# Kernel tuning notes

Hardware: AMD Instinct MI355X
Metric: run time of the kernel (lower is better)

The kernel has to match this reference:

```python
import jax, jax.numpy as jnp
import numpy as np
import math

B, S, E, H = 4, 1024, 1024, 16
DK = E // H  # 64


def setup_inputs() -> dict:
    key = jax.random.key(0)
    ks = jax.random.split(key, 10)
    sc = 0.02
    inp = {
        "x": jax.random.normal(ks[0], (B, S, E), dtype=jnp.float32),
        "mask": jax.random.randint(ks[1], (B, S, S), 0, 2, dtype=jnp.int32),
        "Wq": jax.random.normal(ks[2], (E, E), dtype=jnp.float32) * sc,
        "bq": jnp.zeros((E,), dtype=jnp.float32),
        "Wk": jax.random.normal(ks[3], (E, E), dtype=jnp.float32) * sc,
        "bk": jnp.zeros((E,), dtype=jnp.float32),
        "Wv": jax.random.normal(ks[4], (E, E), dtype=jnp.float32) * sc,
        "bv": jnp.zeros((E,), dtype=jnp.float32),
        "Wo": jax.random.normal(ks[5], (E, E), dtype=jnp.float32) * sc,
        "bo": jnp.zeros((E,), dtype=jnp.float32),
    }
    return inp


def _split_heads(t):
    # [B, S, E] -> [B, H, S, DK]
    return t.reshape(B, S, H, DK).transpose(0, 2, 1, 3)


def reference(x, mask, Wq, bq, Wk, bk, Wv, bv, Wo, bo):
    # Linear projections (torch Linear: y = x @ W.T + b)
    q = _split_heads(x @ Wq.T + bq)
    k = _split_heads(x @ Wk.T + bk)
    v = _split_heads(x @ Wv.T + bv)  # computed but discarded, faithful to source bug
    # scores: [B, H, S, S]
    scores = jnp.einsum('bhqd,bhkd->bhqk', q, k) / jnp.float32(math.sqrt(DK))
    scores = jnp.where(mask[:, None, :, :] == 0, jnp.float32(-1e9), scores)
    scores = jax.nn.softmax(scores, axis=-1)
    # NOTE: source forward keeps dropout(scores) (eval mode -> identity) and
    # DISCARDS matmul(scores, v). We replicate that exactly.
    attn = scores  # [B, H, S, S]
    attn = attn.transpose(0, 2, 1, 3).reshape(B, -1, E)  # [B, S*S/DK, E]
    return attn @ Wo.T + bo
```

## Files before the change

### kernel.cpp

```cpp
#include <hip/hip_runtime.h>

typedef __bf16 bf16;
typedef __attribute__((ext_vector_type(8))) __bf16 bf16x8;
typedef __attribute__((ext_vector_type(4))) float f32x4;


__device__ __forceinline__ unsigned short f2bf(float f) {
    union { float f; unsigned u; } v; v.f = f;
    unsigned r = v.u + 0x7FFFu + ((v.u >> 16) & 1u);
    return (unsigned short)(r >> 16);
}

__device__ __forceinline__ void stage128x64(const bf16* g, int ld_elems,
                                            bf16* lds, int tid) {
    const char* gb = (const char*)g;
    const int ldb = ld_elems * 2;
#pragma unroll
    for (int r = 0; r < 4; ++r) {
        int lin = r * 256 + tid;
        int row = lin >> 3;
        int ch  = (lin & 7) ^ (row & 7);
        __builtin_amdgcn_global_load_lds(
            (const __attribute__((address_space(1))) void*)(gb + (size_t)row * ldb + ch * 16),
            (__attribute__((address_space(3))) void*)(lds + lin * 8),
            16, 0, 0);
    }
}

__device__ __forceinline__ void stage_half512(const bf16* g, bf16* lds, int tid) {
    const char* gb = (const char*)g;
#pragma unroll
    for (int r = 0; r < 2; ++r) {
        int lin = r * 512 + tid;
        int row = lin >> 3;
        int ch  = (lin & 7) ^ (row & 7);
        __builtin_amdgcn_global_load_lds(
            (const __attribute__((address_space(1))) void*)(gb + (size_t)row * 2048 + ch * 16),
            (__attribute__((address_space(3))) void*)(lds + lin * 8),
            16, 0, 0);
    }
}

__device__ __forceinline__ void mma_tile(const bf16* As, const bf16* Bs,
                                         int wm, int wn, int lane,
                                         f32x4 acc[4][4]) {
    const int lm = lane & 15;
    const int g  = lane >> 4;
#pragma unroll
    for (int ks = 0; ks < 2; ++ks) {
        const int c = ks * 4 + g;
        bf16x8 a[4], b[4];
#pragma unroll
        for (int t = 0; t < 4; ++t) {
            const int row = wm * 64 + t * 16 + lm;
            a[t] = *(const bf16x8*)(As + row * 64 + ((c ^ (row & 7)) << 3));
        }
#pragma unroll
        for (int t = 0; t < 4; ++t) {
            const int row = wn * 64 + t * 16 + lm;
            b[t] = *(const bf16x8*)(Bs + row * 64 + ((c ^ (row & 7)) << 3));
        }
#pragma unroll
        for (int i = 0; i < 4; ++i)
#pragma unroll
            for (int j = 0; j < 4; ++j)
                acc[i][j] = __builtin_amdgcn_mfma_f32_16x16x32_bf16(a[i], b[j], acc[i][j], 0, 0, 0);
    }
}


__global__ void convert_kernel(const float* __restrict__ x,  const float* __restrict__ Wq,
                               const float* __restrict__ Wk, const float* __restrict__ Wo,
                               unsigned short* xb, unsigned short* Wqb,
                               unsigned short* Wkb, unsigned short* Wob) {
    size_t i = ((size_t)blockIdx.x * 256 + threadIdx.x) * 4;
    const float* src; unsigned short* dst; size_t off;
    if      (i < 4194304) { src = x;  dst = xb;  off = i; }
    else if (i < 5242880) { src = Wq; dst = Wqb; off = i - 4194304; }
    else if (i < 6291456) { src = Wk; dst = Wkb; off = i - 5242880; }
    else                  { src = Wo; dst = Wob; off = i - 6291456; }
    float4 v = *(const float4*)(src + off);
    ushort4 o;
    o.x = f2bf(v.x); o.y = f2bf(v.y); o.z = f2bf(v.z); o.w = f2bf(v.w);
    *(ushort4*)(dst + off) = o;
}

__global__ __launch_bounds__(256) void proj_kernel(
        const bf16* __restrict__ X, const bf16* __restrict__ Wqb,
        const bf16* __restrict__ Wkb, const float* __restrict__ bq,
        const float* __restrict__ bk, unsigned short* Qb, unsigned short* Kb) {
    __shared__ bf16 As[128 * 64];
    __shared__ bf16 Bs[128 * 64];
    const int tid = threadIdx.x, wid = tid >> 6, lane = tid & 63;
    const int wm = wid >> 1, wn = wid & 1;
    const int n0 = blockIdx.x * 128, m0 = blockIdx.y * 128;
    const bf16*  W    = blockIdx.z ? Wkb : Wqb;
    const float* bias = blockIdx.z ? bk  : bq;
    unsigned short* Out = blockIdx.z ? Kb : Qb;

    f32x4 acc[4][4];
    const f32x4 z4 = {0.f, 0.f, 0.f, 0.f};
#pragma unroll
    for (int i = 0; i < 4; ++i)
#pragma unroll
        for (int j = 0; j < 4; ++j) acc[i][j] = z4;

    for (int kt = 0; kt < 16; ++kt) {
        stage128x64(X + (size_t)m0 * 1024 + kt * 64, 1024, As, tid);
        stage128x64(W + (size_t)n0 * 1024 + kt * 64, 1024, Bs, tid);
        __syncthreads();
        mma_tile(As, Bs, wm, wn, lane, acc);
        __syncthreads();
    }

    const int q = lane >> 4, lm = lane & 15;
#pragma unroll
    for (int j = 0; j < 4; ++j) {
        const int col = n0 + wn * 64 + j * 16 + lm;
        const float bc = bias[col];
#pragma unroll
        for (int i = 0; i < 4; ++i)
#pragma unroll
            for (int r = 0; r < 4; ++r) {
                const int row = m0 + wm * 64 + i * 16 + q * 4 + r;
                Out[(size_t)row * 1024 + col] = f2bf(acc[i][j][r] + bc);
            }
    }
}

__global__ __launch_bounds__(256) void scores_kernel(
        const bf16* __restrict__ Qb, const bf16* __restrict__ Kb,
        const int* __restrict__ mask, unsigned short* Pun, float* Z) {
    __shared__ bf16 As[128 * 64];
    __shared__ bf16 Bs[2][128 * 64];
    __shared__ float Zs[2][128];
    const int tid = threadIdx.x, wid = tid >> 6, lane = tid & 63;
    const int wm = wid >> 1, wn = wid & 1;
    const int i0 = blockIdx.x * 128;
    const int h = blockIdx.y & 15, b = blockIdx.y >> 4;
    const int q = lane >> 4, lm = lane & 15;

    const bf16* Qh = Qb + ((size_t)(b * 1024 + i0)) * 1024 + h * 64;
    const bf16* Kh = Kb + ((size_t)(b * 1024)) * 1024 + h * 64;

    stage128x64(Qh, 1024, As, tid);
    stage128x64(Kh, 1024, Bs[0], tid);

    float rs[4][4];
#pragma unroll
    for (int i = 0; i < 4; ++i)
#pragma unroll
        for (int r = 0; r < 4; ++r) rs[i][r] = 0.f;

    for (int jt = 0; jt < 8; ++jt) {
        __syncthreads();
        if (jt < 7)
            stage128x64(Kh + (size_t)(jt + 1) * 128 * 1024, 1024, Bs[(jt + 1) & 1], tid);

        f32x4 acc[4][4];
        const f32x4 z4 = {0.f, 0.f, 0.f, 0.f};
#pragma unroll
        for (int i = 0; i < 4; ++i)
#pragma unroll
            for (int j = 0; j < 4; ++j) acc[i][j] = z4;
        mma_tile(As, Bs[jt & 1], wm, wn, lane, acc);

#pragma unroll
        for (int i = 0; i < 4; ++i)
#pragma unroll
            for (int r = 0; r < 4; ++r) {
                const int ii = i0 + wm * 64 + i * 16 + q * 4 + r;
                const size_t mrow = (size_t)b * 16384 + (size_t)ii * 16 + h;
#pragma unroll
                for (int j = 0; j < 4; ++j) {
                    const int jj = jt * 128 + wn * 64 + j * 16 + lm;
                    const float s = acc[i][j][r] * 0.125f;
                    const int mk = mask[((size_t)b * 1024 + ii) * 1024 + jj];
                    const float p = mk ? __expf(s) : 0.f;
                    Pun[mrow * 1024 + jj] = f2bf(p);
                    rs[i][r] += p;
                }
            }
    }

#pragma unroll
    for (int i = 0; i < 4; ++i)
#pragma unroll
        for (int r = 0; r < 4; ++r) {
            float v = rs[i][r];
            for (int off = 1; off < 16; off <<= 1) v += __shfl_xor(v, off, 16);
            if (lm == 0) Zs[wn][wm * 64 + i * 16 + q * 4 + r] = v;
        }
    __syncthreads();
    if (tid < 128) {
        const size_t m = (size_t)b * 16384 + (size_t)(i0 + tid) * 16 + h;
        Z[m] = Zs[0][tid] + Zs[1][tid];
    }
}

__global__ __launch_bounds__(512, 2) void out_gemm_kernel(
        const bf16* __restrict__ Pun, const bf16* __restrict__ Wob,
        const float* __restrict__ Z, const float* __restrict__ bo,
        float* __restrict__ out) {
    __shared__ bf16 As[2][2][128 * 64];
    __shared__ bf16 Bs[2][2][128 * 64];
    const int tid = threadIdx.x, wid = tid >> 6, lane = tid & 63;
    const int wm = wid >> 2, wn = wid & 3;
    const int lm = lane & 15, g = lane >> 4;

    const int bx = blockIdx.x, xcd = bx & 7, j = bx >> 3;
    const int m0 = (xcd * 32 + (j >> 2)) * 256;
    const int n0 = (j & 3) * 256;
    const bf16* Apan = Pun + (size_t)m0 * 1024;
    const bf16* Bpan = Wob + (size_t)n0 * 1024;

    f32x4 acc[8][4];
    const f32x4 z4 = {0.f, 0.f, 0.f, 0.f};
#pragma unroll
    for (int mi = 0; mi < 8; ++mi)
#pragma unroll
        for (int nj = 0; nj < 4; ++nj) acc[mi][nj] = z4;

    stage_half512(Bpan,                 Bs[0][0], tid);
    stage_half512(Bpan + 128 * 1024,    Bs[0][1], tid);
    stage_half512(Apan,                 As[0][0], tid);
    stage_half512(Apan + 128 * 1024,    As[0][1], tid);
    stage_half512(Bpan + 64,            Bs[1][0], tid);
    asm volatile("s_waitcnt vmcnt(2)" ::: "memory");
    __builtin_amdgcn_s_barrier();
    __builtin_amdgcn_sched_barrier(0);

    bf16x8 b[4];

#define MFMA16(MH)                                                            \
    _Pragma("unroll")                                                         \
    for (int mi = 0; mi < 4; ++mi)                                            \
      _Pragma("unroll")                                                       \
      for (int nj = 0; nj < 4; ++nj)                                          \
        acc[(MH) * 4 + mi][nj] = __builtin_amdgcn_mfma_f32_16x16x32_bf16(     \
            a[mi], b[nj], acc[(MH) * 4 + mi][nj], 0, 0, 0);

#define PHASE(BUF, MH, KS, RB, STAGE, GATE)                                   \
  {                                                                           \
    const int cs = ((((KS) * 4) + g) ^ (lm & 7)) << 3;                        \
    const bf16* pA = &As[BUF][wm][((MH) * 64 + lm) * 64] + cs;                \
    bf16x8 a[4];                                                              \
    _Pragma("unroll")                                                         \
    for (int mi = 0; mi < 4; ++mi)                                            \
      a[mi] = *(const bf16x8*)(pA + mi * 16 * 64);                            \
    if (RB) {                                                                 \
      const bf16* pB = &Bs[BUF][wn >> 1][((wn & 1) * 64 + lm) * 64] + cs;     \
      _Pragma("unroll")                                                       \
      for (int nj = 0; nj < 4; ++nj)                                          \
        b[nj] = *(const bf16x8*)(pB + nj * 16 * 64);                          \
    }                                                                         \
    STAGE;                                                                    \
    __builtin_amdgcn_s_barrier();                                             \
    asm volatile("s_waitcnt lgkmcnt(0)" ::: "memory");                        \
    __builtin_amdgcn_sched_barrier(0);                                        \
    __builtin_amdgcn_s_setprio(1);                                            \
    MFMA16(MH);                                                               \
    __builtin_amdgcn_s_setprio(0);                                            \
    __builtin_amdgcn_sched_barrier(0);                                        \
    GATE;                                                                     \
    __builtin_amdgcn_s_barrier();                                             \
    __builtin_amdgcn_sched_barrier(0);                                        \
  }

#pragma unroll 1
    for (int t = 0; t < 16; t += 2) {
        const bool more = (t < 14);
        PHASE(0, 0, 0, true,
              stage_half512(Bpan + 128 * 1024 + (t + 1) * 64, Bs[1][1], tid), )
        PHASE(0, 1, 0, false,
              stage_half512(Apan + (t + 1) * 64, As[1][0], tid), )
        PHASE(0, 0, 1, true,
              stage_half512(Apan + 128 * 1024 + (t + 1) * 64, As[1][1], tid), )
        PHASE(0, 1, 1, false,
              if (more) stage_half512(Bpan + (t + 2) * 64, Bs[0][0], tid),
              if (more) { asm volatile("s_waitcnt vmcnt(2)" ::: "memory"); }
              else      { asm volatile("s_waitcnt vmcnt(0)" ::: "memory"); } )
        PHASE(1, 0, 0, true,
              if (more) stage_half512(Bpan + 128 * 1024 + (t + 2) * 64, Bs[0][1], tid), )
        PHASE(1, 1, 0, false,
              if (more) stage_half512(Apan + (t + 2) * 64, As[0][0], tid), )
        PHASE(1, 0, 1, true,
              if (more) stage_half512(Apan + 128 * 1024 + (t + 2) * 64, As[0][1], tid), )
        PHASE(1, 1, 1, false,
              if (more) stage_half512(Bpan + (t + 3) * 64, Bs[1][0], tid),
              if (more) { asm volatile("s_waitcnt vmcnt(2)" ::: "memory"); } )
    }
#undef PHASE
#undef MFMA16

#pragma unroll
    for (int mi = 0; mi < 8; ++mi) {
#pragma unroll
        for (int r = 0; r < 4; ++r) {
            const int row = m0 + wm * 128 + mi * 16 + g * 4 + r;
            const float zi = 1.0f / Z[row];
#pragma unroll
            for (int nj = 0; nj < 4; ++nj) {
                const int col = n0 + wn * 64 + nj * 16 + lm;
                out[(size_t)row * 1024 + col] = acc[mi][nj][r] * zi + bo[col];
            }
        }
    }
}


extern "C" void kernel_launch(void* const* d_in, const int* in_sizes, int n_in,
                              void* d_out, int out_size, void* d_ws, size_t ws_size,
                              hipStream_t stream) {
    (void)in_sizes; (void)n_in; (void)out_size; (void)ws_size;
    const float* x    = (const float*)d_in[0];
    const int*   mask = (const int*)d_in[1];
    const float* Wq   = (const float*)d_in[2];
    const float* bq   = (const float*)d_in[3];
    const float* Wk   = (const float*)d_in[4];
    const float* bk   = (const float*)d_in[5];
    const float* Wo   = (const float*)d_in[8];
    const float* bo   = (const float*)d_in[9];

    char* ws = (char*)d_ws;
    bf16*  xb  = (bf16*)(ws);
    bf16*  Wqb = (bf16*)(ws + 8388608);
    bf16*  Wkb = (bf16*)(ws + 10485760);
    bf16*  Wob = (bf16*)(ws + 12582912);
    bf16*  Qb  = (bf16*)(ws + 14680064);
    bf16*  Kb  = (bf16*)(ws + 23068672);
    float* Z   = (float*)(ws + 31457280);
    bf16*  Pun = (bf16*)(ws + 31981568);

    convert_kernel<<<7168, 256, 0, stream>>>(x, Wq, Wk, Wo,
        (unsigned short*)xb, (unsigned short*)Wqb, (unsigned short*)Wkb,
        (unsigned short*)Wob);
    proj_kernel<<<dim3(8, 32, 2), 256, 0, stream>>>(xb, Wqb, Wkb, bq, bk,
        (unsigned short*)Qb, (unsigned short*)Kb);
    scores_kernel<<<dim3(8, 64), 256, 0, stream>>>(Qb, Kb, mask,
        (unsigned short*)Pun, Z);
    out_gemm_kernel<<<1024, 512, 0, stream>>>(Pun, Wob, Z, bo, (float*)d_out);
}
```

Measured before the change: 547.5 us.

## Load B fragments for both k-substeps at once and deepen prefetch schedule

Each B tile is now read from LDS once per buffer into eight registers covering both k-substeps, so two of the four phases per buffer skip their B reads. The global-to-LDS staging order is rearranged: both halves of the next B tile are issued together, the prologue preloads more tiles, and the vmcnt waits are loosened to allow more loads in flight. The goal is fewer LDS reads and deeper memory-compute overlap, at the cost of more VGPRs for the B fragments and a more fragile wait-count schedule.

```diff
diff --git a/kernel.cpp b/kernel.cpp
--- a/kernel.cpp
+++ b/kernel.cpp
@@ -221,45 +221,51 @@
 #pragma unroll
         for (int nj = 0; nj < 4; ++nj) acc[mi][nj] = z4;
 
-    stage_half512(Bpan,                 Bs[0][0], tid);
-    stage_half512(Bpan + 128 * 1024,    Bs[0][1], tid);
-    stage_half512(Apan,                 As[0][0], tid);
-    stage_half512(Apan + 128 * 1024,    As[0][1], tid);
-    stage_half512(Bpan + 64,            Bs[1][0], tid);
-    asm volatile("s_waitcnt vmcnt(2)" ::: "memory");
+    stage_half512(Bpan,                   Bs[0][0], tid);
+    stage_half512(Bpan + 128 * 1024,      Bs[0][1], tid);
+    stage_half512(Apan,                   As[0][0], tid);
+    stage_half512(Apan + 128 * 1024,      As[0][1], tid);
+    stage_half512(Bpan + 64,              Bs[1][0], tid);
+    stage_half512(Bpan + 128 * 1024 + 64, Bs[1][1], tid);
+    stage_half512(Apan + 64,              As[1][0], tid);
+    asm volatile("s_waitcnt vmcnt(6)" ::: "memory");
     __builtin_amdgcn_s_barrier();
     __builtin_amdgcn_sched_barrier(0);
 
-    bf16x8 b[4];
-
-#define MFMA16(MH)                                                            \
+    bf16x8 b[8];
+
+#define MFMA16(MH, KS)                                                        \
     _Pragma("unroll")                                                         \
     for (int mi = 0; mi < 4; ++mi)                                            \
       _Pragma("unroll")                                                       \
       for (int nj = 0; nj < 4; ++nj)                                          \
         acc[(MH) * 4 + mi][nj] = __builtin_amdgcn_mfma_f32_16x16x32_bf16(     \
-            a[mi], b[nj], acc[(MH) * 4 + mi][nj], 0, 0, 0);
+            a[mi], b[(KS) * 4 + nj], acc[(MH) * 4 + mi][nj], 0, 0, 0);
 
 #define PHASE(BUF, MH, KS, RB, STAGE, GATE)                                   \
   {                                                                           \
-    const int cs = ((((KS) * 4) + g) ^ (lm & 7)) << 3;                        \
-    const bf16* pA = &As[BUF][wm][((MH) * 64 + lm) * 64] + cs;                \
+    const bf16* pA = &As[BUF][wm][((MH) * 64 + lm) * 64];                     \
+    const int csk = (((KS) * 4 + g) ^ (lm & 7)) << 3;                         \
     bf16x8 a[4];                                                              \
     _Pragma("unroll")                                                         \
     for (int mi = 0; mi < 4; ++mi)                                            \
-      a[mi] = *(const bf16x8*)(pA + mi * 16 * 64);                            \
+      a[mi] = *(const bf16x8*)(pA + mi * 16 * 64 + csk);                      \
     if (RB) {                                                                 \
-      const bf16* pB = &Bs[BUF][wn >> 1][((wn & 1) * 64 + lm) * 64] + cs;     \
+      const bf16* pB = &Bs[BUF][wn >> 1][((wn & 1) * 64 + lm) * 64];          \
       _Pragma("unroll")                                                       \
-      for (int nj = 0; nj < 4; ++nj)                                          \
-        b[nj] = *(const bf16x8*)(pB + nj * 16 * 64);                          \
+      for (int k2 = 0; k2 < 2; ++k2) {                                        \
+        const int cs2 = ((k2 * 4 + g) ^ (lm & 7)) << 3;                       \
+        _Pragma("unroll")                                                     \
+        for (int nj = 0; nj < 4; ++nj)                                        \
+          b[k2 * 4 + nj] = *(const bf16x8*)(pB + nj * 16 * 64 + cs2);         \
+      }                                                                       \
     }                                                                         \
     STAGE;                                                                    \
     __builtin_amdgcn_s_barrier();                                             \
     asm volatile("s_waitcnt lgkmcnt(0)" ::: "memory");                        \
     __builtin_amdgcn_sched_barrier(0);                                        \
     __builtin_amdgcn_s_setprio(1);                                            \
-    MFMA16(MH);                                                               \
+    MFMA16(MH, KS);                                                           \
     __builtin_amdgcn_s_setprio(0);                                            \
     __builtin_amdgcn_sched_barrier(0);                                        \
     GATE;                                                                     \
@@ -271,24 +277,24 @@
     for (int t = 0; t < 16; t += 2) {
         const bool more = (t < 14);
         PHASE(0, 0, 0, true,
-              stage_half512(Bpan + 128 * 1024 + (t + 1) * 64, Bs[1][1], tid), )
+              stage_half512(Apan + 128 * 1024 + (t + 1) * 64, As[1][1], tid), )
         PHASE(0, 1, 0, false,
-              stage_half512(Apan + (t + 1) * 64, As[1][0], tid), )
-        PHASE(0, 0, 1, true,
-              stage_half512(Apan + 128 * 1024 + (t + 1) * 64, As[1][1], tid), )
+              if (more) { stage_half512(Bpan + (t + 2) * 64, Bs[0][0], tid);
+                          stage_half512(Bpan + 128 * 1024 + (t + 2) * 64, Bs[0][1], tid); }, )
+        PHASE(0, 0, 1, false, , )
         PHASE(0, 1, 1, false,
-              if (more) stage_half512(Bpan + (t + 2) * 64, Bs[0][0], tid),
-              if (more) { asm volatile("s_waitcnt vmcnt(2)" ::: "memory"); }
+              if (more) stage_half512(Apan + (t + 2) * 64, As[0][0], tid),
+              if (more) { asm volatile("s_waitcnt vmcnt(6)" ::: "memory"); }
               else      { asm volatile("s_waitcnt vmcnt(0)" ::: "memory"); } )
         PHASE(1, 0, 0, true,
-              if (more) stage_half512(Bpan + 128 * 1024 + (t + 2) * 64, Bs[0][1], tid), )
+              if (more) stage_half512(Apan + 128 * 1024 + (t + 2) * 64, As[0][1], tid), )
         PHASE(1, 1, 0, false,
-              if (more) stage_half512(Apan + (t + 2) * 64, As[0][0], tid), )
-        PHASE(1, 0, 1, true,
-              if (more) stage_half512(Apan + 128 * 1024 + (t + 2) * 64, As[0][1], tid), )
+              if (more) { stage_half512(Bpan + (t + 3) * 64, Bs[1][0], tid);
+                          stage_half512(Bpan + 128 * 1024 + (t + 3) * 64, Bs[1][1], tid); }, )
+        PHASE(1, 0, 1, false, , )
         PHASE(1, 1, 1, false,
-              if (more) stage_half512(Bpan + (t + 3) * 64, Bs[1][0], tid),
-              if (more) { asm volatile("s_waitcnt vmcnt(2)" ::: "memory"); } )
+              if (more) stage_half512(Apan + (t + 3) * 64, As[1][0], tid),
+              if (more) { asm volatile("s_waitcnt vmcnt(6)" ::: "memory"); } )
     }
 #undef PHASE
 #undef MFMA16
```

After: 545.9 us. About the same (-0.3%).
